# Kernel optimization log

Measured on AMD Instinct MI355X. Metric: run time of the kernel, lower is better.

Reference implementation:

```python
import jax, jax.numpy as jnp
import numpy as np

SHOT, WAY, DIM, Q, R = 5, 32, 640, 4096, 10
TEMP, L, DIV = 16.0, 2.0, 10.0
EPS = 1e-5


def _expmap0(x, c):
    # x: (..., d); c: broadcastable to (..., 1). Exponential map at origin + ball projection.
    sc = jnp.sqrt(c)
    n = jnp.maximum(jnp.linalg.norm(x, axis=-1, keepdims=True), EPS)
    y = jnp.tanh(sc * n) * x / (sc * n)
    ny = jnp.maximum(jnp.linalg.norm(y, axis=-1, keepdims=True), EPS)
    maxn = (1.0 - 1e-3) / sc
    return jnp.where(ny > maxn, y * (maxn / ny), y)


def _dist(x, y, c):
    # Poincare distance: 2/sqrt(c) * artanh(sqrt(c) * ||mobius_add(-x, y)||)
    u = -x
    uy = jnp.sum(u * y, -1, keepdims=True)
    u2 = jnp.sum(u * u, -1, keepdims=True)
    y2 = jnp.sum(y * y, -1, keepdims=True)
    num = (1.0 + 2.0 * c * uy + c * y2) * u + (1.0 - c * u2) * y
    den = jnp.maximum(1.0 + 2.0 * c * uy + c * c * u2 * y2, EPS)
    n = jnp.linalg.norm(num / den, axis=-1, keepdims=True)
    sc = jnp.sqrt(c)
    arg = jnp.clip(sc * n, 0.0, 1.0 - EPS)
    return ((2.0 / sc) * jnp.arctanh(arg))[..., 0]


def setup_inputs() -> dict:
    key = jax.random.key(0)
    ks = jax.random.split(key, 8)
    f = lambda k, s: jax.random.normal(k, s, dtype=jnp.float32)
    z = lambda s: jnp.zeros(s, jnp.float32)
    return {
        "data_shot": f(ks[0], (SHOT * WAY, DIM)),
        "data_query": f(ks[1], (Q, DIM)),
        "W1": f(ks[2], (2 * DIM, 128)) * 0.05, "b1": z((128,)),
        "W2": f(ks[3], (128, 64)) * 0.05, "b2": z((64,)),
        "W3": f(ks[4], (64, 5)) * 0.05, "b3": z((5,)),
        "Wr1": f(ks[5], (2 * R + 2, R)) * 0.05, "br1": z((R,)),
        "Wr2": f(ks[6], (R, R + 1)) * 0.05, "br2": z((R + 1,)),
    }


def reference(data_shot, data_query, W1, b1, W2, b2, W3, b3, Wr1, br1, Wr2, br2):
    # --- episode stats + per-class curvature controller ---
    all_data = jnp.concatenate([data_shot, data_query], 0).mean(0)      # (dim,)
    protos = data_shot.reshape(SHOT, WAY, DIM).mean(0)                  # (way, dim)
    ctrl_in = jnp.concatenate([protos, jnp.broadcast_to(all_data, (WAY, DIM))], 1)
    h = jax.nn.relu(ctrl_in @ W1 + b1)
    h = jax.nn.relu(h @ W2 + b2)
    cand = jnp.arange(1, 6, dtype=jnp.float32) * (L / DIV)              # 5 curvature candidates
    c = jax.nn.softmax(h @ W3 + b3, axis=-1) @ cand                     # (way,) positive curvature

    # --- hyperbolic projection + per-class proto-query distances (vectorized over classes) ---
    proto_p = _expmap0(protos, c[:, None])                              # (way, dim)
    query_p = _expmap0(data_query[None], c[:, None, None])              # (way, Q, dim)
    dis_mat = _dist(proto_p[:, None, :], query_p, c[:, None, None])     # (way, Q)

    # --- sort + gather-based rerank features ---
    idx = jnp.argsort(dis_mat, axis=1)
    idx_near, idx_far = idx[:, :R], idx[:, R:]
    n_i_d = jnp.take_along_axis(dis_mat, idx_near, 1)                   # (way, R)
    o_i_d = jnp.take_along_axis(dis_mat, idx_far, 1).mean(1)            # (way,)
    dT = dis_mat.T                                                      # (Q, way)
    Gnear = dT[idx_near]                                                # (way, R, way): [i,k,j] = dis_mat[j, idx_near[i,k]]
    n_o_d = (Gnear.sum(-1) - n_i_d) / (WAY - 1)                         # (way, R)
    Gfar = dT[idx_far]                                                  # (way, Q-R, way)
    ii = jnp.arange(WAY)
    mlt = (ii[None, :] < ii[:, None]).astype(dis_mat.dtype)             # j < i
    mgt = (ii[None, :] > ii[:, None]).astype(dis_mat.dtype)             # j > i
    sumA = jnp.einsum('ikj,ij->i', Gfar, mlt)                           # gathered cols (rows before i)
    sumB = mgt @ dis_mat[:, R:].sum(1)                                  # raw cols R: (rows after i, as in source)
    o_o_d = (sumA + sumB) / ((WAY - 1) * (Q - R))

    # --- rerank controller MLP ---
    rr_in = jnp.concatenate([n_i_d, n_o_d, o_i_d[:, None], o_o_d[:, None]], 1)  # (way, 2R+2)
    hr = jax.nn.relu(rr_in @ Wr1 + br1)
    orr = hr @ Wr2 + br2                                                # (way, R+1)
    i_w = jax.nn.softmax(orr[:, :R], axis=-1)                           # (way, R)
    onw = jax.nn.sigmoid(orr[:, R])                                     # (way,)

    # --- proto update + final distances ---
    near_q = data_query[idx_near]                                       # (way, R, dim)
    wdq = (near_q * i_w[:, :, None]).sum(1)                             # (way, dim)
    tmp = protos * onw[:, None] + wdq * (1.0 - onw[:, None])
    test_proto = _expmap0(tmp, c[:, None])
    new_dis = _dist(test_proto[:, None, :], query_p, c[:, None, None])  # (way, Q)
    return -new_dis.T / TEMP                                            # (Q, way)
```

## Files before the change

kernel.cpp:

```cpp
#include <hip/hip_runtime.h>
#include <math.h>

#define NSHOT 5
#define WAY 32
#define DIM 640
#define NQ 4096
#define RNEAR 10

constexpr int OFF_PROTOS = 0;
constexpr int OFF_QPART  = 20480;
constexpr int OFF_C      = 102400;
constexpr int OFF_XVEC   = 102432;
constexpr int OFF_DIS    = 122912;
constexpr int OFF_S      = 253984;
constexpr int OFF_U      = 254016;
constexpr int OFF_NID    = 254048;
constexpr int OFF_TP     = 254368;
constexpr int OFF_NIDX   = 274848;
constexpr int OFF_Q2D    = 275200;
constexpr int OFF_X2D    = 283392;
constexpr int OFF_X2D2   = 283456;

__device__ __forceinline__ double wave_sum_d(double v) {
#pragma unroll
  for (int o = 32; o > 0; o >>= 1) v += __shfl_down(v, o, 64);
  return v;
}

__device__ __forceinline__ double dist_hyp(double c, double xdotq, double u2, double q2) {
  const double EPSd = 1e-5;
  double sc = sqrt(c);
  double nq = sqrt(q2);
  double nf = fmax(nq, EPSd);
  double th = tanh(sc * nf);
  double al = th / (sc * nf);
  double ny = fmax(al * nq, EPSd);
  double mx = 0.999 / sc;
  if (ny > mx) al *= mx / ny;
  double y2 = al * al * q2;
  double uy = -al * xdotq;
  double A = 1.0 + 2.0 * c * uy + c * y2;
  double B = 1.0 - c * u2;
  double den = fmax(1.0 + 2.0 * c * uy + c * c * u2 * y2, EPSd);
  double num2 = fmax(A * A * u2 + 2.0 * A * B * uy + B * B * y2, 0.0);
  double n = sqrt(num2) / den;
  double arg = sc * n;
  const double CLIP = (double)(1.0f - 1e-5f);
  arg = fmin(fmax(arg, 0.0), CLIP);
  return (1.0 / sc) * log((1.0 + arg) / (1.0 - arg));
}

__device__ __forceinline__ double expmap_scale(double c, double p2, double* u2out) {
  double sc = sqrt(c);
  double ntrue = sqrt(p2);
  double nf = fmax(ntrue, 1e-5);
  double th = tanh(sc * nf);
  double s0 = th / (sc * nf);
  double ny = fmax(s0 * ntrue, 1e-5);
  double mx = 0.999 / sc;
  if (ny > mx) s0 *= mx / ny;
  *u2out = s0 * s0 * p2;
  return s0;
}

__global__ __launch_bounds__(640) void k_fuse1(const float* __restrict__ Qm,
                                               const float* __restrict__ shot, float* ws) {
  __shared__ double q2w[32][10];
  int b = blockIdx.x, t = threadIdx.x;
  int lane = t & 63, wid = t >> 6;
  float protoval = 0.f;
  if (b < WAY) {
    float s = 0.f;
#pragma unroll
    for (int s5 = 0; s5 < NSHOT; ++s5) s += shot[(size_t)(s5 * WAY + b) * DIM + t];
    protoval = s * 0.2f;
    ws[OFF_PROTOS + b * DIM + t] = protoval;
  }
  int r0 = b * 32;
  float colacc = 0.f;
  for (int r = 0; r < 32; ++r) {
    float v = Qm[(size_t)(r0 + r) * DIM + t];
    colacc += v;
    double sq = (double)v * v;
    sq = wave_sum_d(sq);
    if (lane == 0) q2w[r][wid] = sq;
  }
  ws[OFF_QPART + b * DIM + t] = colacc + 5.f * protoval;
  __syncthreads();
  if (t < 32) {
    double s = 0.0;
#pragma unroll
    for (int k = 0; k < 10; ++k) s += q2w[t][k];
    ((double*)(ws + OFF_Q2D))[r0 + t] = s;
  }
}

__global__ __launch_bounds__(512) void k_ctrl(const float* __restrict__ W1, const float* __restrict__ b1,
                                              const float* __restrict__ W2, const float* __restrict__ b2,
                                              const float* __restrict__ W3, const float* __restrict__ b3,
                                              float* ws) {
  __shared__ float cat[2 * DIM];
  __shared__ float4 ampart[3][160];
  __shared__ float h1p[16][128];
  __shared__ float h1s[128];
  __shared__ float h2p[8][64], h2s[64];
  __shared__ float lg[5];
  __shared__ double redd[8];
  __shared__ double sBeta;
  int w = blockIdx.x, t = threadIdx.x;
  int lane = t & 63, wid = t >> 6;
  double ps = 0.0;
  for (int d = t; d < DIM; d += 512) {
    float v = ws[OFF_PROTOS + w * DIM + d];
    cat[d] = v; ps += (double)v * v;
  }
  ps = wave_sum_d(ps);
  if (lane == 0) redd[wid] = ps;
  if (t < 480) {
    int s = t / 160, quad = t - s * 160;
    int p0 = s * 43, p1 = (s == 2) ? 128 : (p0 + 43);
    float4 a = {0.f, 0.f, 0.f, 0.f};
#pragma unroll 4
    for (int p = p0; p < p1; ++p) {
      float4 v = *(const float4*)&ws[OFF_QPART + p * DIM + quad * 4];
      a.x += v.x; a.y += v.y; a.z += v.z; a.w += v.w;
    }
    ampart[s][quad] = a;
  }
  __syncthreads();
  if (t < 160) {
    float4 a = ampart[0][t], b4 = ampart[1][t], c4 = ampart[2][t];
    float4 r;
    r.x = (a.x + b4.x + c4.x) / 4256.f;
    r.y = (a.y + b4.y + c4.y) / 4256.f;
    r.z = (a.z + b4.z + c4.z) / 4256.f;
    r.w = (a.w + b4.w + c4.w) / 4256.f;
    *(float4*)&cat[DIM + t * 4] = r;
  }
  __syncthreads();
  {
    int ng = t & 31, ks = t >> 5;
    int k0 = ks * 80;
    float4 acc = {0.f, 0.f, 0.f, 0.f};
#pragma unroll 8
    for (int k = k0; k < k0 + 80; ++k) {
      float4 wr = *(const float4*)&W1[(size_t)k * 128 + ng * 4];
      float xv = cat[k];
      acc.x = fmaf(xv, wr.x, acc.x);
      acc.y = fmaf(xv, wr.y, acc.y);
      acc.z = fmaf(xv, wr.z, acc.z);
      acc.w = fmaf(xv, wr.w, acc.w);
    }
    *(float4*)&h1p[ks][ng * 4] = acc;
  }
  __syncthreads();
  if (t < 128) {
    float a = b1[t];
#pragma unroll
    for (int s = 0; s < 16; ++s) a += h1p[s][t];
    h1s[t] = fmaxf(a, 0.f);
  }
  __syncthreads();
  {
    int n = t & 63, s2 = t >> 6;
    int k0 = s2 * 16;
    float acc = 0.f;
#pragma unroll
    for (int k = 0; k < 16; ++k) acc = fmaf(h1s[k0 + k], W2[(size_t)(k0 + k) * 64 + n], acc);
    h2p[s2][n] = acc;
  }
  __syncthreads();
  if (t < 64) {
    float a = b2[t];
#pragma unroll
    for (int s = 0; s < 8; ++s) a += h2p[s][t];
    h2s[t] = fmaxf(a, 0.f);
  }
  __syncthreads();
  if (t < 5) {
    float a = b3[t];
    for (int k = 0; k < 64; ++k) a = fmaf(h2s[k], W3[k * 5 + t], a);
    lg[t] = a;
  }
  __syncthreads();
  if (t == 0) {
    double p2 = 0.0;
    for (int i = 0; i < 8; ++i) p2 += redd[i];
    double m = lg[0];
    for (int i = 1; i < 5; ++i) m = fmax(m, (double)lg[i]);
    double se = 0.0, cv = 0.0;
    for (int i = 0; i < 5; ++i) { double e = exp((double)lg[i] - m); se += e; cv += e * 0.2 * (double)(i + 1); }
    double c = cv / se;
    ws[OFF_C + w] = (float)c;
    double u2;
    sBeta = expmap_scale(c, p2, &u2);
    ((double*)(ws + OFF_X2D))[w] = u2;
  }
  __syncthreads();
  float beta = (float)sBeta;
  for (int d = t; d < DIM; d += 512) ws[OFF_XVEC + w * DIM + d] = beta * cat[d];
}

__global__ __launch_bounds__(256) void k_gemmdist(const float* __restrict__ X, const float* __restrict__ Qm,
                                                  float* __restrict__ ws, int mode, float* __restrict__ out) {
  __shared__ float S[2][40][68];
  int t = threadIdx.x;
  int q0 = blockIdx.x * 8;
  int rowA = t >> 4, quadA = t & 15;
  int rowB = (t + 256) >> 4;
  int rowC = (t + 512) >> 4;
  bool hasC = (t < 128);
  const float* srcA = (rowA < 8 ? Qm + (size_t)(q0 + rowA) * DIM : X + (size_t)(rowA - 8) * DIM) + quadA * 4;
  const float* srcB = X + (size_t)(rowB - 8) * DIM + quadA * 4;
  const float* srcC = X + (size_t)(rowC - 8) * DIM + quadA * 4;
  float4 pA = *(const float4*)srcA;
  float4 pB = *(const float4*)srcB;
  float4 pC = {0.f, 0.f, 0.f, 0.f};
  if (hasC) pC = *(const float4*)srcC;
  *(float4*)&S[0][rowA][quadA * 4] = pA;
  *(float4*)&S[0][rowB][quadA * 4] = pB;
  if (hasC) *(float4*)&S[0][rowC][quadA * 4] = pC;
  __syncthreads();
  int q = t & 7, w = t >> 3;
  float ax = 0.f, ay = 0.f, az = 0.f, aw = 0.f;
  for (int c = 0; c < 10; ++c) {
    int bsel = c & 1;
    if (c < 9) {
      size_t kc = (size_t)(c + 1) * 64;
      pA = *(const float4*)(srcA + kc);
      pB = *(const float4*)(srcB + kc);
      if (hasC) pC = *(const float4*)(srcC + kc);
    }
    const float* qr = &S[bsel][q][0];
    const float* xr = &S[bsel][8 + w][0];
#pragma unroll
    for (int kk = 0; kk < 64; kk += 4) {
      float4 qv = *(const float4*)(qr + kk);
      float4 xv = *(const float4*)(xr + kk);
      ax = fmaf(qv.x, xv.x, ax);
      ay = fmaf(qv.y, xv.y, ay);
      az = fmaf(qv.z, xv.z, az);
      aw = fmaf(qv.w, xv.w, aw);
    }
    if (c < 9) {
      int nb = bsel ^ 1;
      *(float4*)&S[nb][rowA][quadA * 4] = pA;
      *(float4*)&S[nb][rowB][quadA * 4] = pB;
      if (hasC) *(float4*)&S[nb][rowC][quadA * 4] = pC;
      __syncthreads();
    }
  }
  float acc = (ax + ay) + (az + aw);
  const double* q2d   = (const double*)(ws + OFF_Q2D);
  const double* u2arr = (const double*)(ws + (mode ? OFF_X2D2 : OFF_X2D));
  int qq = q0 + q;
  double d = dist_hyp((double)ws[OFF_C + w], (double)acc, u2arr[w], q2d[qq]);
  if (mode == 0) {
    ws[OFF_DIS + (size_t)w * NQ + qq] = (float)d;
  } else {
    out[(size_t)qq * WAY + w] = (float)(-d / 16.0);
  }
}

__global__ __launch_bounds__(1024) void k_topk(float* ws, int* nidx) {
  __shared__ double sredS[16], sredU[16];
  __shared__ float cval[160];
  __shared__ int cidx[160];
  int w = blockIdx.x, t = threadIdx.x;
  int lane = t & 63, wid = t >> 6;
  const float* base = ws + OFF_DIS + (size_t)w * NQ;
  float v0 = base[t], v1 = base[1024 + t], v2 = base[2048 + t], v3 = base[3072 + t];
  unsigned tk = 0;
  double s = (double)v0 + (double)v1 + (double)v2 + (double)v3;
  double u = (t < RNEAR) ? (double)v0 : 0.0;
  s = wave_sum_d(s);
  u = wave_sum_d(u);
  if (lane == 0) { sredS[wid] = s; sredU[wid] = u; }
  for (int r = 0; r < RNEAR; ++r) {
    float lv = INFINITY; int li = 0x7fffffff;
    if (!(tk & 1u) && (v0 < lv || (v0 == lv && t < li)))        { lv = v0; li = t; }
    if (!(tk & 2u) && (v1 < lv || (v1 == lv && 1024 + t < li))) { lv = v1; li = 1024 + t; }
    if (!(tk & 4u) && (v2 < lv || (v2 == lv && 2048 + t < li))) { lv = v2; li = 2048 + t; }
    if (!(tk & 8u) && (v3 < lv || (v3 == lv && 3072 + t < li))) { lv = v3; li = 3072 + t; }
#pragma unroll
    for (int o = 32; o > 0; o >>= 1) {
      float ov = __shfl_xor(lv, o, 64);
      int oi = __shfl_xor(li, o, 64);
      if (ov < lv || (ov == lv && oi < li)) { lv = ov; li = oi; }
    }
    if (lane == 0) { cval[wid * RNEAR + r] = lv; cidx[wid * RNEAR + r] = li; }
    if ((li & 1023) == t) tk |= 1u << (li >> 10);
  }
  __syncthreads();
  if (t == 0) {
    double S = 0.0, U = 0.0;
    for (int k = 0; k < 16; ++k) { S += sredS[k]; U += sredU[k]; }
    ws[OFF_S + w] = (float)S;
    ws[OFF_U + w] = (float)U;
  }
  if (t < 64) {
    float c0 = cval[t], c1 = cval[t + 64];
    int i0 = cidx[t], i1 = cidx[t + 64];
    float c2 = (t < 32) ? cval[t + 128] : INFINITY;
    int i2 = (t < 32) ? cidx[t + 128] : 0x7fffffff;
    unsigned m = 0;
    for (int r = 0; r < RNEAR; ++r) {
      float lv = INFINITY; int li = 0x7fffffff;
      if (!(m & 1u) && (c0 < lv || (c0 == lv && i0 < li))) { lv = c0; li = i0; }
      if (!(m & 2u) && (c1 < lv || (c1 == lv && i1 < li))) { lv = c1; li = i1; }
      if (!(m & 4u) && (c2 < lv || (c2 == lv && i2 < li))) { lv = c2; li = i2; }
#pragma unroll
      for (int o = 32; o > 0; o >>= 1) {
        float ov = __shfl_xor(lv, o, 64);
        int oi = __shfl_xor(li, o, 64);
        if (ov < lv || (ov == lv && oi < li)) { lv = ov; li = oi; }
      }
      if (lane == 0) {
        ws[OFF_NID + w * RNEAR + r] = lv;
        nidx[w * RNEAR + r] = li;
      }
      if (i0 == li) m |= 1u;
      if (i1 == li) m |= 2u;
      if (i2 == li) m |= 4u;
    }
  }
}

__global__ __launch_bounds__(512) void k_reftmp(const float* __restrict__ Qm,
                                                const float* __restrict__ Wr1, const float* __restrict__ br1,
                                                const float* __restrict__ Wr2, const float* __restrict__ br2,
                                                float* ws, const int* __restrict__ nidx) {
  __shared__ float colsh[RNEAR][33];
  __shared__ float rr[22];
  __shared__ float qjNid[RNEAR];
  __shared__ int qj[RNEAR];
  __shared__ float Ssh[WAY], Ush[WAY];
  __shared__ float hr[RNEAR], iw[RNEAR];
  __shared__ float onw_sh;
  __shared__ double p2red[8];
  __shared__ double gshd;
  int w = blockIdx.x, t = threadIdx.x;
  int lane = t & 63, wid = t >> 6;
  if (t < WAY) { Ssh[t] = ws[OFF_S + t]; Ush[t] = ws[OFF_U + t]; }
  if (t >= 64 && t < 64 + RNEAR) {
    int j = t - 64;
    qj[j] = nidx[w * RNEAR + j];
    qjNid[j] = ws[OFF_NID + w * RNEAR + j];
  }
  __syncthreads();
  if (t < WAY * RNEAR) {
    int j = t >> 5, w2 = t & 31;
    colsh[j][w2] = ws[OFF_DIS + (size_t)w2 * NQ + qj[j]];
  }
  __syncthreads();
  if (t < RNEAR) {
    double cs = 0.0, pc = 0.0;
    for (int w2 = 0; w2 < WAY; ++w2) {
      float dv = colsh[t][w2];
      cs += dv;
      if (w2 < w) pc += dv;
    }
    rr[t] = qjNid[t];
    rr[RNEAR + t] = (float)((cs - qjNid[t]) / (double)(WAY - 1));
    colsh[t][32] = (float)pc;
  }
  __syncthreads();
  if (t == 0) {
    double sn = 0.0; for (int j = 0; j < RNEAR; ++j) sn += rr[j];
    double oi = ((double)Ssh[w] - sn) / (double)(NQ - RNEAR);
    double pref = 0.0; for (int j = 0; j < w; ++j) pref += Ssh[j];
    double suf = 0.0; for (int j = w + 1; j < WAY; ++j) suf += (double)Ssh[j] - (double)Ush[j];
    double spc = 0.0; for (int j = 0; j < RNEAR; ++j) spc += colsh[j][32];
    rr[20] = (float)oi;
    rr[21] = (float)((pref - spc + suf) / ((double)(WAY - 1) * (double)(NQ - RNEAR)));
  }
  __syncthreads();
  if (t < RNEAR) {
    float a = br1[t];
    for (int k = 0; k < 22; ++k) a = fmaf(rr[k], Wr1[k * RNEAR + t], a);
    hr[t] = fmaxf(a, 0.f);
  }
  __syncthreads();
  if (t == 0) {
    double o[11];
    for (int r2 = 0; r2 < 11; ++r2) {
      float a = br2[r2];
      for (int k = 0; k < RNEAR; ++k) a = fmaf(hr[k], Wr2[k * 11 + r2], a);
      o[r2] = a;
    }
    double m = o[0]; for (int i = 1; i < RNEAR; ++i) m = fmax(m, o[i]);
    double se = 0.0; double e[RNEAR];
    for (int i = 0; i < RNEAR; ++i) { e[i] = exp(o[i] - m); se += e[i]; }
    for (int i = 0; i < RNEAR; ++i) iw[i] = (float)(e[i] / se);
    onw_sh = (float)(1.0 / (1.0 + exp(-o[10])));
  }
  __syncthreads();
  float onwv = onw_sh;
  float a0 = 0.f, a1 = 0.f;
  bool has2 = (t + 512 < DIM);
  double ls = 0.0;
  {
    int d = t;
    float wd = 0.f;
#pragma unroll
    for (int j = 0; j < RNEAR; ++j) wd = fmaf(Qm[(size_t)qj[j] * DIM + d], iw[j], wd);
    a0 = ws[OFF_PROTOS + w * DIM + d] * onwv + wd * (1.f - onwv);
    ls += (double)a0 * a0;
  }
  if (has2) {
    int d = t + 512;
    float wd = 0.f;
#pragma unroll
    for (int j = 0; j < RNEAR; ++j) wd = fmaf(Qm[(size_t)qj[j] * DIM + d], iw[j], wd);
    a1 = ws[OFF_PROTOS + w * DIM + d] * onwv + wd * (1.f - onwv);
    ls += (double)a1 * a1;
  }
  ls = wave_sum_d(ls);
  if (lane == 0) p2red[wid] = ls;
  __syncthreads();
  if (t == 0) {
    double p2 = 0.0;
    for (int i = 0; i < 8; ++i) p2 += p2red[i];
    double c = (double)ws[OFF_C + w];
    double u2;
    gshd = expmap_scale(c, p2, &u2);
    ((double*)(ws + OFF_X2D2))[w] = u2;
  }
  __syncthreads();
  float g = (float)gshd;
  ws[OFF_TP + w * DIM + t] = g * a0;
  if (has2) ws[OFF_TP + w * DIM + t + 512] = g * a1;
}

extern "C" void kernel_launch(void* const* d_in, const int* in_sizes, int n_in,
                              void* d_out, int out_size, void* d_ws, size_t ws_size,
                              hipStream_t stream) {
  (void)in_sizes; (void)n_in; (void)out_size; (void)ws_size;
  const float* shot = (const float*)d_in[0];
  const float* qry  = (const float*)d_in[1];
  const float* W1   = (const float*)d_in[2];
  const float* b1   = (const float*)d_in[3];
  const float* W2   = (const float*)d_in[4];
  const float* b2   = (const float*)d_in[5];
  const float* W3   = (const float*)d_in[6];
  const float* b3   = (const float*)d_in[7];
  const float* Wr1  = (const float*)d_in[8];
  const float* br1  = (const float*)d_in[9];
  const float* Wr2  = (const float*)d_in[10];
  const float* br2  = (const float*)d_in[11];
  float* ws = (float*)d_ws;
  float* out = (float*)d_out;
  int* nidx = (int*)(ws + OFF_NIDX);

  hipLaunchKernelGGL(k_fuse1,    dim3(128), dim3(640), 0, stream, qry, shot, ws);
  hipLaunchKernelGGL(k_ctrl,     dim3(32), dim3(512), 0, stream, W1, b1, W2, b2, W3, b3, ws);
  hipLaunchKernelGGL(k_gemmdist, dim3(512), dim3(256), 0, stream, ws + OFF_XVEC, qry, ws, 0, out);
  hipLaunchKernelGGL(k_topk,     dim3(32), dim3(1024), 0, stream, ws, nidx);
  hipLaunchKernelGGL(k_reftmp,   dim3(32), dim3(512), 0, stream, qry, Wr1, br1, Wr2, br2, ws, nidx);
  hipLaunchKernelGGL(k_gemmdist, dim3(512), dim3(256), 0, stream, ws + OFF_TP, qry, ws, 1, out);
}
```

Measured before the change: 86.85 us.

## Fuse pipeline into four kernels with raw-dot GEMM and last-block reduction

```diff
diff --git a/kernel.cpp b/kernel.cpp
--- a/kernel.cpp
+++ b/kernel.cpp
@@ -10,21 +10,33 @@
 constexpr int OFF_PROTOS = 0;
 constexpr int OFF_QPART  = 20480;
 constexpr int OFF_C      = 102400;
-constexpr int OFF_XVEC   = 102432;
-constexpr int OFF_DIS    = 122912;
-constexpr int OFF_S      = 253984;
-constexpr int OFF_U      = 254016;
-constexpr int OFF_NID    = 254048;
-constexpr int OFF_TP     = 254368;
-constexpr int OFF_NIDX   = 274848;
-constexpr int OFF_Q2D    = 275200;
-constexpr int OFF_X2D    = 283392;
-constexpr int OFF_X2D2   = 283456;
+constexpr int OFF_BETA   = 102432;
+constexpr int OFF_S      = 102464;
+constexpr int OFF_U      = 102496;
+constexpr int OFF_NID    = 102528;
+constexpr int OFF_RR     = 102848;
+constexpr int OFF_SPC    = 103552;
+constexpr int OFF_H1P    = 103584;
+constexpr int OFF_TP     = 107680;
+constexpr int OFF_G      = 128160;
+constexpr int OFF_NIDX   = 259232;
+constexpr int OFF_CNT    = 259552;
+constexpr int OFF_Q2D    = 259556;
+constexpr int OFF_X2D    = 267748;
+constexpr int OFF_X2D2   = 267812;
+constexpr int OFF_P2RAW  = 267876;
 
 __device__ __forceinline__ double wave_sum_d(double v) {
 #pragma unroll
   for (int o = 32; o > 0; o >>= 1) v += __shfl_down(v, o, 64);
   return v;
+}
+
+__device__ __forceinline__ float aloadf(const float* p) {
+  return __hip_atomic_load(p, __ATOMIC_RELAXED, __HIP_MEMORY_SCOPE_AGENT);
+}
+__device__ __forceinline__ int aloadi(const int* p) {
+  return __hip_atomic_load(p, __ATOMIC_RELAXED, __HIP_MEMORY_SCOPE_AGENT);
 }
 
 __device__ __forceinline__ double dist_hyp(double c, double xdotq, double u2, double q2) {
@@ -64,8 +76,12 @@
 }
 
 __global__ __launch_bounds__(640) void k_fuse1(const float* __restrict__ Qm,
-                                               const float* __restrict__ shot, float* ws) {
+                                               const float* __restrict__ shot,
+                                               const float* __restrict__ W1, float* ws) {
   __shared__ double q2w[32][10];
+  __shared__ double psred[10];
+  __shared__ float pr[DIM];
+  __shared__ float h1pp[5][128];
   int b = blockIdx.x, t = threadIdx.x;
   int lane = t & 63, wid = t >> 6;
   float protoval = 0.f;
@@ -74,7 +90,11 @@
 #pragma unroll
     for (int s5 = 0; s5 < NSHOT; ++s5) s += shot[(size_t)(s5 * WAY + b) * DIM + t];
     protoval = s * 0.2f;
+    pr[t] = protoval;
     ws[OFF_PROTOS + b * DIM + t] = protoval;
+    double pv2 = (double)protoval * protoval;
+    pv2 = wave_sum_d(pv2);
+    if (lane == 0) psred[wid] = pv2;
   }
   int r0 = b * 32;
   float colacc = 0.f;
@@ -93,117 +113,356 @@
     for (int k = 0; k < 10; ++k) s += q2w[t][k];
     ((double*)(ws + OFF_Q2D))[r0 + t] = s;
   }
-}
-
-__global__ __launch_bounds__(512) void k_ctrl(const float* __restrict__ W1, const float* __restrict__ b1,
-                                              const float* __restrict__ W2, const float* __restrict__ b2,
-                                              const float* __restrict__ W3, const float* __restrict__ b3,
-                                              float* ws) {
-  __shared__ float cat[2 * DIM];
-  __shared__ float4 ampart[3][160];
-  __shared__ float h1p[16][128];
-  __shared__ float h1s[128];
-  __shared__ float h2p[8][64], h2s[64];
-  __shared__ float lg[5];
-  __shared__ double redd[8];
-  __shared__ double sBeta;
+  if (b < WAY) {
+    int n = t & 127, s = t >> 7;
+    int k0 = s * 128;
+    float acc = 0.f;
+#pragma unroll 8
+    for (int k = k0; k < k0 + 128; ++k) acc = fmaf(pr[k], W1[(size_t)k * 128 + n], acc);
+    h1pp[s][n] = acc;
+    __syncthreads();
+    if (t < 128)
+      ws[OFF_H1P + b * 128 + t] = h1pp[0][t] + h1pp[1][t] + h1pp[2][t] + h1pp[3][t] + h1pp[4][t];
+    if (t == 0) {
+      double p2 = 0.0;
+#pragma unroll
+      for (int k = 0; k < 10; ++k) p2 += psred[k];
+      ((double*)(ws + OFF_P2RAW))[b] = p2;
+    }
+  }
+  if (b == 0 && t == 0) ((int*)(ws + OFF_CNT))[0] = 0;
+}
+
+struct GemmSm { float S[2][40][68]; };
+struct CtrlSm {
+  float am[DIM];
+  float part[2][128];
+  float h1s[WAY][128];
+  float h2s[WAY][64];
+  float lg[WAY][5];
+};
+union Sm1 { GemmSm g; CtrlSm c; };
+
+__global__ __launch_bounds__(256) void k_gemm1(const float* __restrict__ Qm,
+                                               const float* __restrict__ W1, const float* __restrict__ b1,
+                                               const float* __restrict__ W2, const float* __restrict__ b2,
+                                               const float* __restrict__ W3, const float* __restrict__ b3,
+                                               float* __restrict__ ws) {
+  __shared__ Sm1 sm;
+  int t = threadIdx.x;
+  if (blockIdx.x < 512) {
+    const float* X = ws + OFF_PROTOS;
+    int q0 = blockIdx.x * 8;
+    int rowA = t >> 4, quadA = t & 15;
+    int rowB = (t + 256) >> 4;
+    int rowC = (t + 512) >> 4;
+    bool hasC = (t < 128);
+    const float* srcA = (rowA < 8 ? Qm + (size_t)(q0 + rowA) * DIM : X + (size_t)(rowA - 8) * DIM) + quadA * 4;
+    const float* srcB = X + (size_t)(rowB - 8) * DIM + quadA * 4;
+    const float* srcC = X + (size_t)(rowC - 8) * DIM + quadA * 4;
+    float4 pA = *(const float4*)srcA;
+    float4 pB = *(const float4*)srcB;
+    float4 pC = {0.f, 0.f, 0.f, 0.f};
+    if (hasC) pC = *(const float4*)srcC;
+    *(float4*)&sm.g.S[0][rowA][quadA * 4] = pA;
+    *(float4*)&sm.g.S[0][rowB][quadA * 4] = pB;
+    if (hasC) *(float4*)&sm.g.S[0][rowC][quadA * 4] = pC;
+    __syncthreads();
+    int q = t & 7, w = t >> 3;
+    float ax = 0.f, ay = 0.f, az = 0.f, aw = 0.f;
+    for (int c = 0; c < 10; ++c) {
+      int bsel = c & 1;
+      if (c < 9) {
+        size_t kc = (size_t)(c + 1) * 64;
+        pA = *(const float4*)(srcA + kc);
+        pB = *(const float4*)(srcB + kc);
+        if (hasC) pC = *(const float4*)(srcC + kc);
+      }
+      const float* qr = &sm.g.S[bsel][q][0];
+      const float* xr = &sm.g.S[bsel][8 + w][0];
+#pragma unroll
+      for (int kk = 0; kk < 64; kk += 4) {
+        float4 qv = *(const float4*)(qr + kk);
+        float4 xv = *(const float4*)(xr + kk);
+        ax = fmaf(qv.x, xv.x, ax);
+        ay = fmaf(qv.y, xv.y, ay);
+        az = fmaf(qv.z, xv.z, az);
+        aw = fmaf(qv.w, xv.w, aw);
+      }
+      if (c < 9) {
+        int nb = bsel ^ 1;
+        *(float4*)&sm.g.S[nb][rowA][quadA * 4] = pA;
+        *(float4*)&sm.g.S[nb][rowB][quadA * 4] = pB;
+        if (hasC) *(float4*)&sm.g.S[nb][rowC][quadA * 4] = pC;
+        __syncthreads();
+      }
+    }
+    ws[OFF_G + (size_t)w * NQ + q0 + q] = (ax + ay) + (az + aw);
+  } else {
+    if (t < 160) {
+      float4 a = {0.f, 0.f, 0.f, 0.f};
+#pragma unroll 4
+      for (int p = 0; p < 128; ++p) {
+        float4 v = *(const float4*)&ws[OFF_QPART + p * DIM + t * 4];
+        a.x += v.x; a.y += v.y; a.z += v.z; a.w += v.w;
+      }
+      sm.c.am[t * 4 + 0] = a.x / 4256.f;
+      sm.c.am[t * 4 + 1] = a.y / 4256.f;
+      sm.c.am[t * 4 + 2] = a.z / 4256.f;
+      sm.c.am[t * 4 + 3] = a.w / 4256.f;
+    }
+    __syncthreads();
+    {
+      int n = t & 127, s = t >> 7;
+      int k0 = s * 320;
+      float acc = 0.f;
+#pragma unroll 8
+      for (int k = k0; k < k0 + 320; ++k)
+        acc = fmaf(sm.c.am[k], W1[(size_t)(DIM + k) * 128 + n], acc);
+      sm.c.part[s][n] = acc;
+    }
+    __syncthreads();
+#pragma unroll
+    for (int i = 0; i < 16; ++i) {
+      int idx = i * 256 + t;
+      int w = idx >> 7, n = idx & 127;
+      sm.c.h1s[w][n] = fmaxf(ws[OFF_H1P + w * 128 + n] + sm.c.part[0][n] + sm.c.part[1][n] + b1[n], 0.f);
+    }
+    __syncthreads();
+#pragma unroll
+    for (int i = 0; i < 8; ++i) {
+      int idx = i * 256 + t;
+      int w = idx >> 6, n = idx & 63;
+      float acc = 0.f;
+      for (int k = 0; k < 128; ++k) acc = fmaf(sm.c.h1s[w][k], W2[(size_t)k * 64 + n], acc);
+      sm.c.h2s[w][n] = fmaxf(acc + b2[n], 0.f);
+    }
+    __syncthreads();
+    if (t < 160) {
+      int w = t / 5, j = t - (t / 5) * 5;
+      float acc = b3[j];
+      for (int k = 0; k < 64; ++k) acc = fmaf(sm.c.h2s[w][k], W3[k * 5 + j], acc);
+      sm.c.lg[w][j] = acc;
+    }
+    __syncthreads();
+    if (t < WAY) {
+      double m = sm.c.lg[t][0];
+      for (int i = 1; i < 5; ++i) m = fmax(m, (double)sm.c.lg[t][i]);
+      double se = 0.0, cv = 0.0;
+      for (int i = 0; i < 5; ++i) { double e = exp((double)sm.c.lg[t][i] - m); se += e; cv += e * 0.2 * (double)(i + 1); }
+      double c = cv / se;
+      ws[OFF_C + t] = (float)c;
+      double p2 = ((const double*)(ws + OFF_P2RAW))[t];
+      double u2;
+      double beta = expmap_scale(c, p2, &u2);
+      ws[OFF_BETA + t] = (float)beta;
+      ((double*)(ws + OFF_X2D))[t] = u2;
+    }
+  }
+}
+
+__global__ __launch_bounds__(1024) void k_topkref(const float* __restrict__ Qm,
+                                                  const float* __restrict__ Wr1, const float* __restrict__ br1,
+                                                  const float* __restrict__ Wr2, const float* __restrict__ br2,
+                                                  float* __restrict__ ws) {
+  __shared__ double sredS[16], sredU[16];
+  __shared__ float cval[160];
+  __shared__ int cidx[160];
+  __shared__ float qvsh[RNEAR];
+  __shared__ int qjsh[RNEAR];
+  __shared__ float colsh[RNEAR][33];
+  __shared__ float pcpart[RNEAR];
+  __shared__ int tailflag;
+  __shared__ float rrsh[WAY][22];
+  __shared__ float hrsh[WAY][RNEAR];
+  __shared__ float orsh[WAY][11];
+  __shared__ float iwsh[WAY][RNEAR];
+  __shared__ float onwsh[WAY];
+  __shared__ int nidxsh[WAY][RNEAR];
+  __shared__ double p2sh[WAY];
+  __shared__ float gsh[WAY];
+
   int w = blockIdx.x, t = threadIdx.x;
   int lane = t & 63, wid = t >> 6;
-  double ps = 0.0;
-  for (int d = t; d < DIM; d += 512) {
-    float v = ws[OFF_PROTOS + w * DIM + d];
-    cat[d] = v; ps += (double)v * v;
-  }
-  ps = wave_sum_d(ps);
-  if (lane == 0) redd[wid] = ps;
-  if (t < 480) {
-    int s = t / 160, quad = t - s * 160;
-    int p0 = s * 43, p1 = (s == 2) ? 128 : (p0 + 43);
-    float4 a = {0.f, 0.f, 0.f, 0.f};
-#pragma unroll 4
-    for (int p = p0; p < p1; ++p) {
-      float4 v = *(const float4*)&ws[OFF_QPART + p * DIM + quad * 4];
-      a.x += v.x; a.y += v.y; a.z += v.z; a.w += v.w;
-    }
-    ampart[s][quad] = a;
-  }
-  __syncthreads();
-  if (t < 160) {
-    float4 a = ampart[0][t], b4 = ampart[1][t], c4 = ampart[2][t];
-    float4 r;
-    r.x = (a.x + b4.x + c4.x) / 4256.f;
-    r.y = (a.y + b4.y + c4.y) / 4256.f;
-    r.z = (a.z + b4.z + c4.z) / 4256.f;
-    r.w = (a.w + b4.w + c4.w) / 4256.f;
-    *(float4*)&cat[DIM + t * 4] = r;
+  int* nidx = (int*)(ws + OFF_NIDX);
+  const double* q2d = (const double*)(ws + OFF_Q2D);
+  const double* x2d = (const double*)(ws + OFF_X2D);
+  double c = (double)ws[OFF_C + w];
+  double beta = (double)ws[OFF_BETA + w];
+  double u2 = x2d[w];
+  const float* gb = ws + OFF_G + (size_t)w * NQ;
+  float v0 = (float)dist_hyp(c, beta * (double)gb[t],        u2, q2d[t]);
+  float v1 = (float)dist_hyp(c, beta * (double)gb[1024 + t], u2, q2d[1024 + t]);
+  float v2 = (float)dist_hyp(c, beta * (double)gb[2048 + t], u2, q2d[2048 + t]);
+  float v3 = (float)dist_hyp(c, beta * (double)gb[3072 + t], u2, q2d[3072 + t]);
+  unsigned tk = 0;
+  double s = (double)v0 + (double)v1 + (double)v2 + (double)v3;
+  double u = (t < RNEAR) ? (double)v0 : 0.0;
+  s = wave_sum_d(s);
+  u = wave_sum_d(u);
+  if (lane == 0) { sredS[wid] = s; sredU[wid] = u; }
+  for (int r = 0; r < RNEAR; ++r) {
+    float lv = INFINITY; int li = 0x7fffffff;
+    if (!(tk & 1u) && (v0 < lv || (v0 == lv && t < li)))        { lv = v0; li = t; }
+    if (!(tk & 2u) && (v1 < lv || (v1 == lv && 1024 + t < li))) { lv = v1; li = 1024 + t; }
+    if (!(tk & 4u) && (v2 < lv || (v2 == lv && 2048 + t < li))) { lv = v2; li = 2048 + t; }
+    if (!(tk & 8u) && (v3 < lv || (v3 == lv && 3072 + t < li))) { lv = v3; li = 3072 + t; }
+#pragma unroll
+    for (int o = 32; o > 0; o >>= 1) {
+      float ov = __shfl_xor(lv, o, 64);
+      int oi = __shfl_xor(li, o, 64);
+      if (ov < lv || (ov == lv && oi < li)) { lv = ov; li = oi; }
+    }
+    if (lane == 0) { cval[wid * RNEAR + r] = lv; cidx[wid * RNEAR + r] = li; }
+    if ((li & 1023) == t) tk |= 1u << (li >> 10);
+  }
+  __syncthreads();
+  if (t == 0) {
+    double S = 0.0, U = 0.0;
+    for (int k = 0; k < 16; ++k) { S += sredS[k]; U += sredU[k]; }
+    ws[OFF_S + w] = (float)S;
+    ws[OFF_U + w] = (float)U;
+  }
+  if (t < 64) {
+    float c0 = cval[t], c1 = cval[t + 64];
+    int i0 = cidx[t], i1 = cidx[t + 64];
+    float c2 = (t < 32) ? cval[t + 128] : INFINITY;
+    int i2 = (t < 32) ? cidx[t + 128] : 0x7fffffff;
+    unsigned m = 0;
+    for (int r = 0; r < RNEAR; ++r) {
+      float lv = INFINITY; int li = 0x7fffffff;
+      if (!(m & 1u) && (c0 < lv || (c0 == lv && i0 < li))) { lv = c0; li = i0; }
+      if (!(m & 2u) && (c1 < lv || (c1 == lv && i1 < li))) { lv = c1; li = i1; }
+      if (!(m & 4u) && (c2 < lv || (c2 == lv && i2 < li))) { lv = c2; li = i2; }
+#pragma unroll
+      for (int o = 32; o > 0; o >>= 1) {
+        float ov = __shfl_xor(lv, o, 64);
+        int oi = __shfl_xor(li, o, 64);
+        if (ov < lv || (ov == lv && oi < li)) { lv = ov; li = oi; }
+      }
+      if (lane == 0) {
+        ws[OFF_NID + w * RNEAR + r] = lv;
+        nidx[w * RNEAR + r] = li;
+        qvsh[r] = lv; qjsh[r] = li;
+      }
+      if (i0 == li) m |= 1u;
+      if (i1 == li) m |= 2u;
+      if (i2 == li) m |= 4u;
+    }
+  }
+  __syncthreads();
+  if (t < WAY * RNEAR) {
+    int j = t >> 5, w2 = t & 31;
+    int q = qjsh[j];
+    double c2_ = (double)ws[OFF_C + w2];
+    double b2_ = (double)ws[OFF_BETA + w2];
+    colsh[j][w2] = (float)dist_hyp(c2_, b2_ * (double)ws[OFF_G + (size_t)w2 * NQ + q], x2d[w2], q2d[q]);
+  }
+  __syncthreads();
+  if (t < RNEAR) {
+    double cs = 0.0, pc = 0.0;
+    for (int w2 = 0; w2 < WAY; ++w2) {
+      float dv = colsh[t][w2];
+      cs += dv;
+      if (w2 < w) pc += dv;
+    }
+    ws[OFF_RR + w * 22 + t] = qvsh[t];
+    ws[OFF_RR + w * 22 + RNEAR + t] = (float)((cs - qvsh[t]) / (double)(WAY - 1));
+    pcpart[t] = (float)pc;
+  }
+  __syncthreads();
+  if (t == 0) {
+    double spc = 0.0, sn = 0.0;
+    for (int j = 0; j < RNEAR; ++j) { spc += pcpart[j]; sn += qvsh[j]; }
+    double S = (double)ws[OFF_S + w];
+    ws[OFF_RR + w * 22 + 20] = (float)((S - sn) / (double)(NQ - RNEAR));
+    ws[OFF_SPC + w] = (float)spc;
+  }
+  __threadfence();
+  __syncthreads();
+  if (t == 0) {
+    int old = atomicAdd((int*)(ws + OFF_CNT), 1);
+    tailflag = (old == WAY - 1);
+  }
+  __syncthreads();
+  if (!tailflag) return;
+  __threadfence();
+  for (int i = t; i < WAY * 21; i += 1024) {
+    int ww = i / 21, k = i - ww * 21;
+    rrsh[ww][k] = aloadf(ws + OFF_RR + ww * 22 + k);
+  }
+  for (int i = t; i < WAY * RNEAR; i += 1024) {
+    int ww = i / RNEAR, j = i - ww * RNEAR;
+    nidxsh[ww][j] = aloadi(nidx + ww * RNEAR + j);
+  }
+  if (t < WAY) {
+    double pref = 0.0, suf = 0.0;
+    for (int j = 0; j < t; ++j) pref += (double)aloadf(ws + OFF_S + j);
+    for (int j = t + 1; j < WAY; ++j) suf += (double)aloadf(ws + OFF_S + j) - (double)aloadf(ws + OFF_U + j);
+    double spc = (double)aloadf(ws + OFF_SPC + t);
+    rrsh[t][21] = (float)((pref - spc + suf) / ((double)(WAY - 1) * (double)(NQ - RNEAR)));
+  }
+  __syncthreads();
+  if (t < WAY * RNEAR) {
+    int ww = t / RNEAR, r = t - (t / RNEAR) * RNEAR;
+    float a = br1[r];
+    for (int k = 0; k < 22; ++k) a = fmaf(rrsh[ww][k], Wr1[k * RNEAR + r], a);
+    hrsh[ww][r] = fmaxf(a, 0.f);
+  }
+  __syncthreads();
+  if (t < WAY * 11) {
+    int ww = t / 11, r = t - (t / 11) * 11;
+    float a = br2[r];
+    for (int k = 0; k < RNEAR; ++k) a = fmaf(hrsh[ww][k], Wr2[k * 11 + r], a);
+    orsh[ww][r] = a;
+  }
+  __syncthreads();
+  if (t < WAY) {
+    double m = orsh[t][0];
+    for (int i = 1; i < RNEAR; ++i) m = fmax(m, (double)orsh[t][i]);
+    double se = 0.0; double e[RNEAR];
+    for (int i = 0; i < RNEAR; ++i) { e[i] = exp((double)orsh[t][i] - m); se += e[i]; }
+    for (int i = 0; i < RNEAR; ++i) iwsh[t][i] = (float)(e[i] / se);
+    onwsh[t] = (float)(1.0 / (1.0 + exp(-(double)orsh[t][10])));
   }
   __syncthreads();
   {
-    int ng = t & 31, ks = t >> 5;
-    int k0 = ks * 80;
-    float4 acc = {0.f, 0.f, 0.f, 0.f};
-#pragma unroll 8
-    for (int k = k0; k < k0 + 80; ++k) {
-      float4 wr = *(const float4*)&W1[(size_t)k * 128 + ng * 4];
-      float xv = cat[k];
-      acc.x = fmaf(xv, wr.x, acc.x);
-      acc.y = fmaf(xv, wr.y, acc.y);
-      acc.z = fmaf(xv, wr.z, acc.z);
-      acc.w = fmaf(xv, wr.w, acc.w);
-    }
-    *(float4*)&h1p[ks][ng * 4] = acc;
-  }
-  __syncthreads();
-  if (t < 128) {
-    float a = b1[t];
-#pragma unroll
-    for (int s = 0; s < 16; ++s) a += h1p[s][t];
-    h1s[t] = fmaxf(a, 0.f);
-  }
-  __syncthreads();
-  {
-    int n = t & 63, s2 = t >> 6;
-    int k0 = s2 * 16;
-    float acc = 0.f;
-#pragma unroll
-    for (int k = 0; k < 16; ++k) acc = fmaf(h1s[k0 + k], W2[(size_t)(k0 + k) * 64 + n], acc);
-    h2p[s2][n] = acc;
-  }
-  __syncthreads();
-  if (t < 64) {
-    float a = b2[t];
-#pragma unroll
-    for (int s = 0; s < 8; ++s) a += h2p[s][t];
-    h2s[t] = fmaxf(a, 0.f);
-  }
-  __syncthreads();
-  if (t < 5) {
-    float a = b3[t];
-    for (int k = 0; k < 64; ++k) a = fmaf(h2s[k], W3[k * 5 + t], a);
-    lg[t] = a;
-  }
-  __syncthreads();
-  if (t == 0) {
-    double p2 = 0.0;
-    for (int i = 0; i < 8; ++i) p2 += redd[i];
-    double m = lg[0];
-    for (int i = 1; i < 5; ++i) m = fmax(m, (double)lg[i]);
-    double se = 0.0, cv = 0.0;
-    for (int i = 0; i < 5; ++i) { double e = exp((double)lg[i] - m); se += e; cv += e * 0.2 * (double)(i + 1); }
-    double c = cv / se;
-    ws[OFF_C + w] = (float)c;
-    double u2;
-    sBeta = expmap_scale(c, p2, &u2);
-    ((double*)(ws + OFF_X2D))[w] = u2;
-  }
-  __syncthreads();
-  float beta = (float)sBeta;
-  for (int d = t; d < DIM; d += 512) ws[OFF_XVEC + w * DIM + d] = beta * cat[d];
-}
-
-__global__ __launch_bounds__(256) void k_gemmdist(const float* __restrict__ X, const float* __restrict__ Qm,
-                                                  float* __restrict__ ws, int mode, float* __restrict__ out) {
+    int ww = t >> 5, l = t & 31;
+    float onwv = onwsh[ww];
+    float areg[20];
+    double ls = 0.0;
+#pragma unroll
+    for (int i = 0; i < 20; ++i) {
+      int d = l + i * 32;
+      float wd = 0.f;
+#pragma unroll
+      for (int j = 0; j < RNEAR; ++j)
+        wd = fmaf(Qm[(size_t)nidxsh[ww][j] * DIM + d], iwsh[ww][j], wd);
+      float a = ws[OFF_PROTOS + ww * DIM + d] * onwv + wd * (1.f - onwv);
+      areg[i] = a;
+      ls += (double)a * a;
+    }
+#pragma unroll
+    for (int o = 16; o > 0; o >>= 1) ls += __shfl_xor(ls, o, 32);
+    if (l == 0) p2sh[ww] = ls;
+    __syncthreads();
+    if (t < WAY) {
+      double u22;
+      double g = expmap_scale((double)ws[OFF_C + t], p2sh[t], &u22);
+      gsh[t] = (float)g;
+      ((double*)(ws + OFF_X2D2))[t] = u22;
+    }
+    __syncthreads();
+    float g = gsh[ww];
+#pragma unroll
+    for (int i = 0; i < 20; ++i) ws[OFF_TP + ww * DIM + l + i * 32] = g * areg[i];
+  }
+}
+
+__global__ __launch_bounds__(256) void k_gemm2(const float* __restrict__ Qm,
+                                               float* __restrict__ ws, float* __restrict__ out) {
   __shared__ float S[2][40][68];
+  const float* X = ws + OFF_TP;
   int t = threadIdx.x;
   int q0 = blockIdx.x * 8;
   int rowA = t >> 4, quadA = t & 15;
@@ -251,185 +510,11 @@
     }
   }
   float acc = (ax + ay) + (az + aw);
-  const double* q2d   = (const double*)(ws + OFF_Q2D);
-  const double* u2arr = (const double*)(ws + (mode ? OFF_X2D2 : OFF_X2D));
+  const double* q2d = (const double*)(ws + OFF_Q2D);
+  const double* u2arr = (const double*)(ws + OFF_X2D2);
   int qq = q0 + q;
   double d = dist_hyp((double)ws[OFF_C + w], (double)acc, u2arr[w], q2d[qq]);
-  if (mode == 0) {
-    ws[OFF_DIS + (size_t)w * NQ + qq] = (float)d;
-  } else {
-    out[(size_t)qq * WAY + w] = (float)(-d / 16.0);
-  }
-}
-
-__global__ __launch_bounds__(1024) void k_topk(float* ws, int* nidx) {
-  __shared__ double sredS[16], sredU[16];
-  __shared__ float cval[160];
-  __shared__ int cidx[160];
-  int w = blockIdx.x, t = threadIdx.x;
-  int lane = t & 63, wid = t >> 6;
-  const float* base = ws + OFF_DIS + (size_t)w * NQ;
-  float v0 = base[t], v1 = base[1024 + t], v2 = base[2048 + t], v3 = base[3072 + t];
-  unsigned tk = 0;
-  double s = (double)v0 + (double)v1 + (double)v2 + (double)v3;
-  double u = (t < RNEAR) ? (double)v0 : 0.0;
-  s = wave_sum_d(s);
-  u = wave_sum_d(u);
-  if (lane == 0) { sredS[wid] = s; sredU[wid] = u; }
-  for (int r = 0; r < RNEAR; ++r) {
-    float lv = INFINITY; int li = 0x7fffffff;
-    if (!(tk & 1u) && (v0 < lv || (v0 == lv && t < li)))        { lv = v0; li = t; }
-    if (!(tk & 2u) && (v1 < lv || (v1 == lv && 1024 + t < li))) { lv = v1; li = 1024 + t; }
-    if (!(tk & 4u) && (v2 < lv || (v2 == lv && 2048 + t < li))) { lv = v2; li = 2048 + t; }
-    if (!(tk & 8u) && (v3 < lv || (v3 == lv && 3072 + t < li))) { lv = v3; li = 3072 + t; }
-#pragma unroll
-    for (int o = 32; o > 0; o >>= 1) {
-      float ov = __shfl_xor(lv, o, 64);
-      int oi = __shfl_xor(li, o, 64);
-      if (ov < lv || (ov == lv && oi < li)) { lv = ov; li = oi; }
-    }
-    if (lane == 0) { cval[wid * RNEAR + r] = lv; cidx[wid * RNEAR + r] = li; }
-    if ((li & 1023) == t) tk |= 1u << (li >> 10);
-  }
-  __syncthreads();
-  if (t == 0) {
-    double S = 0.0, U = 0.0;
-    for (int k = 0; k < 16; ++k) { S += sredS[k]; U += sredU[k]; }
-    ws[OFF_S + w] = (float)S;
-    ws[OFF_U + w] = (float)U;
-  }
-  if (t < 64) {
-    float c0 = cval[t], c1 = cval[t + 64];
-    int i0 = cidx[t], i1 = cidx[t + 64];
-    float c2 = (t < 32) ? cval[t + 128] : INFINITY;
-    int i2 = (t < 32) ? cidx[t + 128] : 0x7fffffff;
-    unsigned m = 0;
-    for (int r = 0; r < RNEAR; ++r) {
-      float lv = INFINITY; int li = 0x7fffffff;
-      if (!(m & 1u) && (c0 < lv || (c0 == lv && i0 < li))) { lv = c0; li = i0; }
-      if (!(m & 2u) && (c1 < lv || (c1 == lv && i1 < li))) { lv = c1; li = i1; }
-      if (!(m & 4u) && (c2 < lv || (c2 == lv && i2 < li))) { lv = c2; li = i2; }
-#pragma unroll
-      for (int o = 32; o > 0; o >>= 1) {
-        float ov = __shfl_xor(lv, o, 64);
-        int oi = __shfl_xor(li, o, 64);
-        if (ov < lv || (ov == lv && oi < li)) { lv = ov; li = oi; }
-      }
-      if (lane == 0) {
-        ws[OFF_NID + w * RNEAR + r] = lv;
-        nidx[w * RNEAR + r] = li;
-      }
-      if (i0 == li) m |= 1u;
-      if (i1 == li) m |= 2u;
-      if (i2 == li) m |= 4u;
-    }
-  }
-}
-
-__global__ __launch_bounds__(512) void k_reftmp(const float* __restrict__ Qm,
-                                                const float* __restrict__ Wr1, const float* __restrict__ br1,
-                                                const float* __restrict__ Wr2, const float* __restrict__ br2,
-                                                float* ws, const int* __restrict__ nidx) {
-  __shared__ float colsh[RNEAR][33];
-  __shared__ float rr[22];
-  __shared__ float qjNid[RNEAR];
-  __shared__ int qj[RNEAR];
-  __shared__ float Ssh[WAY], Ush[WAY];
-  __shared__ float hr[RNEAR], iw[RNEAR];
-  __shared__ float onw_sh;
-  __shared__ double p2red[8];
-  __shared__ double gshd;
-  int w = blockIdx.x, t = threadIdx.x;
-  int lane = t & 63, wid = t >> 6;
-  if (t < WAY) { Ssh[t] = ws[OFF_S + t]; Ush[t] = ws[OFF_U + t]; }
-  if (t >= 64 && t < 64 + RNEAR) {
-    int j = t - 64;
-    qj[j] = nidx[w * RNEAR + j];
-    qjNid[j] = ws[OFF_NID + w * RNEAR + j];
-  }
-  __syncthreads();
-  if (t < WAY * RNEAR) {
-    int j = t >> 5, w2 = t & 31;
-    colsh[j][w2] = ws[OFF_DIS + (size_t)w2 * NQ + qj[j]];
-  }
-  __syncthreads();
-  if (t < RNEAR) {
-    double cs = 0.0, pc = 0.0;
-    for (int w2 = 0; w2 < WAY; ++w2) {
-      float dv = colsh[t][w2];
-      cs += dv;
-      if (w2 < w) pc += dv;
-    }
-    rr[t] = qjNid[t];
-    rr[RNEAR + t] = (float)((cs - qjNid[t]) / (double)(WAY - 1));
-    colsh[t][32] = (float)pc;
-  }
-  __syncthreads();
-  if (t == 0) {
-    double sn = 0.0; for (int j = 0; j < RNEAR; ++j) sn += rr[j];
-    double oi = ((double)Ssh[w] - sn) / (double)(NQ - RNEAR);
-    double pref = 0.0; for (int j = 0; j < w; ++j) pref += Ssh[j];
-    double suf = 0.0; for (int j = w + 1; j < WAY; ++j) suf += (double)Ssh[j] - (double)Ush[j];
-    double spc = 0.0; for (int j = 0; j < RNEAR; ++j) spc += colsh[j][32];
-    rr[20] = (float)oi;
-    rr[21] = (float)((pref - spc + suf) / ((double)(WAY - 1) * (double)(NQ - RNEAR)));
-  }
-  __syncthreads();
-  if (t < RNEAR) {
-    float a = br1[t];
-    for (int k = 0; k < 22; ++k) a = fmaf(rr[k], Wr1[k * RNEAR + t], a);
-    hr[t] = fmaxf(a, 0.f);
-  }
-  __syncthreads();
-  if (t == 0) {
-    double o[11];
-    for (int r2 = 0; r2 < 11; ++r2) {
-      float a = br2[r2];
-      for (int k = 0; k < RNEAR; ++k) a = fmaf(hr[k], Wr2[k * 11 + r2], a);
-      o[r2] = a;
-    }
-    double m = o[0]; for (int i = 1; i < RNEAR; ++i) m = fmax(m, o[i]);
-    double se = 0.0; double e[RNEAR];
-    for (int i = 0; i < RNEAR; ++i) { e[i] = exp(o[i] - m); se += e[i]; }
-    for (int i = 0; i < RNEAR; ++i) iw[i] = (float)(e[i] / se);
-    onw_sh = (float)(1.0 / (1.0 + exp(-o[10])));
-  }
-  __syncthreads();
-  float onwv = onw_sh;
-  float a0 = 0.f, a1 = 0.f;
-  bool has2 = (t + 512 < DIM);
-  double ls = 0.0;
-  {
-    int d = t;
-    float wd = 0.f;
-#pragma unroll
-    for (int j = 0; j < RNEAR; ++j) wd = fmaf(Qm[(size_t)qj[j] * DIM + d], iw[j], wd);
-    a0 = ws[OFF_PROTOS + w * DIM + d] * onwv + wd * (1.f - onwv);
-    ls += (double)a0 * a0;
-  }
-  if (has2) {
-    int d = t + 512;
-    float wd = 0.f;
-#pragma unroll
-    for (int j = 0; j < RNEAR; ++j) wd = fmaf(Qm[(size_t)qj[j] * DIM + d], iw[j], wd);
-    a1 = ws[OFF_PROTOS + w * DIM + d] * onwv + wd * (1.f - onwv);
-    ls += (double)a1 * a1;
-  }
-  ls = wave_sum_d(ls);
-  if (lane == 0) p2red[wid] = ls;
-  __syncthreads();
-  if (t == 0) {
-    double p2 = 0.0;
-    for (int i = 0; i < 8; ++i) p2 += p2red[i];
-    double c = (double)ws[OFF_C + w];
-    double u2;
-    gshd = expmap_scale(c, p2, &u2);
-    ((double*)(ws + OFF_X2D2))[w] = u2;
-  }
-  __syncthreads();
-  float g = (float)gshd;
-  ws[OFF_TP + w * DIM + t] = g * a0;
-  if (has2) ws[OFF_TP + w * DIM + t + 512] = g * a1;
+  out[(size_t)qq * WAY + w] = (float)(-d / 16.0);
 }
 
 extern "C" void kernel_launch(void* const* d_in, const int* in_sizes, int n_in,
@@ -450,12 +535,9 @@
   const float* br2  = (const float*)d_in[11];
   float* ws = (float*)d_ws;
   float* out = (float*)d_out;
-  int* nidx = (int*)(ws + OFF_NIDX);
-
-  hipLaunchKernelGGL(k_fuse1,    dim3(128), dim3(640), 0, stream, qry, shot, ws);
-  hipLaunchKernelGGL(k_ctrl,     dim3(32), dim3(512), 0, stream, W1, b1, W2, b2, W3, b3, ws);
-  hipLaunchKernelGGL(k_gemmdist, dim3(512), dim3(256), 0, stream, ws + OFF_XVEC, qry, ws, 0, out);
-  hipLaunchKernelGGL(k_topk,     dim3(32), dim3(1024), 0, stream, ws, nidx);
-  hipLaunchKernelGGL(k_reftmp,   dim3(32), dim3(512), 0, stream, qry, Wr1, br1, Wr2, br2, ws, nidx);
-  hipLaunchKernelGGL(k_gemmdist, dim3(512), dim3(256), 0, stream, ws + OFF_TP, qry, ws, 1, out);
-}
+
+  hipLaunchKernelGGL(k_fuse1,   dim3(128), dim3(640), 0, stream, qry, shot, W1, ws);
+  hipLaunchKernelGGL(k_gemm1,   dim3(513), dim3(256), 0, stream, qry, W1, b1, W2, b2, W3, b3, ws);
+  hipLaunchKernelGGL(k_topkref, dim3(32), dim3(1024), 0, stream, qry, Wr1, br1, Wr2, br2, ws);
+  hipLaunchKernelGGL(k_gemm2,   dim3(512), dim3(256), 0, stream, qry, ws, out);
+}
```

Result: slower. 135.0 us (+55.4%).
